# Optimization experiments

Hardware: AMD Instinct MI355X
Metric: run time of the kernel (lower is better)

The kernel has to match this reference:

```python
import jax, jax.numpy as jnp
import numpy as np

N, DIM, K = 131072, 64, 1024


def setup_inputs() -> dict:
    key = jax.random.key(0)
    kx, ke = jax.random.split(key)
    x = jax.random.normal(kx, (N, DIM), dtype=jnp.float32)
    # codebook buffer, initialized like uniform(-1/K, 1/K) in the original
    scale = 1.0 / K
    embedding = jax.random.uniform(ke, (K, DIM), dtype=jnp.float32, minval=-scale, maxval=scale)
    return {"x": x, "embedding": embedding}


def reference(x, embedding):
    # squared euclidean distances in fp32 (matches compute_distances)
    x32 = x.astype(jnp.float32)
    e32 = embedding.astype(jnp.float32)
    distances = (
        jnp.sum(x32 * x32, axis=1, keepdims=True)
        + jnp.sum(e32 * e32, axis=1)
        - 2.0 * jnp.einsum("nd,kd->nk", x32, e32)
    )
    indices = jnp.argmin(distances, axis=1)          # (N,)
    quantized = embedding[indices]                    # (N, DIM) codebook gather
    # commitment loss: mse(stop_grad(quantized), x)
    commitment_loss = jnp.mean((jax.lax.stop_gradient(quantized) - x) ** 2)
    # straight-through estimator
    quantized_st = x + jax.lax.stop_gradient(quantized - x)
    return quantized_st, indices, commitment_loss
```

## Files before the change

kernel.cpp:

```cpp
#include <hip/hip_runtime.h>
#include <hip/hip_bf16.h>

#define N_ROWS 131072
#define DIM 64
#define K_CODES 1024
#define NTILES 64
#define MARGIN 4e-5f
#define LIST_CAP 65536

typedef short short8 __attribute__((ext_vector_type(8)));
typedef float f32x4 __attribute__((ext_vector_type(4)));

__device__ __forceinline__ unsigned short f2bf(float f) {
    unsigned u = __float_as_uint(f);
    return (unsigned short)((u + 0x7fffu + ((u >> 16) & 1u)) >> 16);
}
__device__ __forceinline__ float bf2f(unsigned short h) {
    return __uint_as_float(((unsigned)h) << 16);
}

__device__ __forceinline__ float np_sq64(const float* __restrict__ v) {
    float xx[DIM];
    #pragma unroll
    for (int d = 0; d < DIM; ++d) xx[d] = v[d] * v[d];
    float r[8];
    #pragma unroll
    for (int j = 0; j < 8; ++j) r[j] = xx[j];
    #pragma unroll
    for (int i = 8; i < DIM; i += 8)
        #pragma unroll
        for (int j = 0; j < 8; ++j) r[j] = r[j] + xx[i + j];
    return ((r[0]+r[1]) + (r[2]+r[3])) + ((r[4]+r[5]) + (r[6]+r[7]));
}

__device__ __forceinline__ float np_dot64(const float* __restrict__ xv,
                                          const float* __restrict__ ek) {
    float a0 = 0.f, a1 = 0.f, a2 = 0.f, a3 = 0.f;
    #pragma unroll
    for (int c = 0; c < DIM; c += 16)
        #pragma unroll
        for (int b = 12; b >= 0; b -= 4) {
            const int d = c + b;
            a0 = a0 + xv[d+0] * ek[d+0];
            a1 = a1 + xv[d+1] * ek[d+1];
            a2 = a2 + xv[d+2] * ek[d+2];
            a3 = a3 + xv[d+3] * ek[d+3];
        }
    return (a0 + a1) + (a2 + a3);
}


__global__ void vq_prep(const float* __restrict__ emb, float* __restrict__ esq,
                        unsigned short* __restrict__ wsB,
                        unsigned int* __restrict__ cnt, float* __restrict__ loss) {
#pragma clang fp contract(off)
    const int t = blockIdx.x * blockDim.x + threadIdx.x;
    if (t == 0) { *cnt = 0u; *loss = 0.f; }
    const int k = t >> 2, c = t & 3;
    if (k >= K_CODES) return;
    const float* e = emb + (size_t)k * DIM;

    if (c == 0) esq[k] = np_sq64(e);

    const int off = (c & 1) * 32, sel = c >> 1;
    unsigned short val[32];
    #pragma unroll
    for (int j = 0; j < 32; ++j) {
        float v = e[off + j];
        unsigned short h = f2bf(v);
        val[j] = sel ? f2bf(v - bf2f(h)) : h;
    }
    const int tile = k >> 4, n = k & 15;
    #pragma unroll
    for (int g = 0; g < 4; ++g) {
        short8 s;
        #pragma unroll
        for (int j = 0; j < 8; ++j) s[j] = (short)val[g*8 + j];
        *reinterpret_cast<short8*>(wsB + ((size_t)((tile*4 + c)*64 + g*16 + n)) * 8) = s;
    }
}

__global__ __launch_bounds__(256, 2) void vq_mfma(const float* __restrict__ x,
        const float* __restrict__ emb, const float* __restrict__ esq,
        const unsigned short* __restrict__ wsB, float* __restrict__ out,
        unsigned int* __restrict__ cnt, unsigned int* __restrict__ list,
        float* __restrict__ loss) {
#pragma clang fp contract(off)
    const int tid = threadIdx.x;
    const int lane = tid & 63;
    const int w = tid >> 6;
    const int g = lane >> 4, res = lane & 15;
    const int rowbase = blockIdx.x * 256 + w * 64;

    short8 Ah[4][2], Al[4][2];
    #pragma unroll
    for (int rg = 0; rg < 4; ++rg) {
        const float* xr = x + (size_t)(rowbase + rg*16 + res) * DIM;
        #pragma unroll
        for (int h = 0; h < 2; ++h) {
            float4 v0 = *reinterpret_cast<const float4*>(xr + h*32 + g*8);
            float4 v1 = *reinterpret_cast<const float4*>(xr + h*32 + g*8 + 4);
            float xv[8] = {v0.x, v0.y, v0.z, v0.w, v1.x, v1.y, v1.z, v1.w};
            short8 sh, sl;
            #pragma unroll
            for (int j = 0; j < 8; ++j) {
                unsigned short hb = f2bf(xv[j]);
                sh[j] = (short)hb;
                sl[j] = (short)f2bf(xv[j] - bf2f(hb));
            }
            Ah[rg][h] = sh; Al[rg][h] = sl;
        }
    }

    float b1[16], b2[16], b3[16];
    const float FINF = __uint_as_float(0x7F800000u);
    #pragma unroll
    for (int s = 0; s < 16; ++s) { b1[s] = FINF; b2[s] = FINF; b3[s] = FINF; }

    auto loadB = [&](short8* Bd, int ct) {
        const unsigned short* bp = wsB + ((size_t)(ct*4)*64 + lane) * 8;
        #pragma unroll
        for (int c = 0; c < 4; ++c)
            Bd[c] = *reinterpret_cast<const short8*>(bp + (size_t)c * 64 * 8);
    };

    auto MF = [&](f32x4* acc, const short8* B) {
        #pragma unroll
        for (int rg = 0; rg < 4; ++rg) acc[rg] = f32x4{0.f, 0.f, 0.f, 0.f};
        #pragma unroll
        for (int rg = 0; rg < 4; ++rg)
            acc[rg] = __builtin_amdgcn_mfma_f32_16x16x32_bf16(Ah[rg][0], B[0], acc[rg], 0,0,0);
        #pragma unroll
        for (int rg = 0; rg < 4; ++rg)
            acc[rg] = __builtin_amdgcn_mfma_f32_16x16x32_bf16(Ah[rg][1], B[1], acc[rg], 0,0,0);
        #pragma unroll
        for (int rg = 0; rg < 4; ++rg)
            acc[rg] = __builtin_amdgcn_mfma_f32_16x16x32_bf16(Ah[rg][0], B[2], acc[rg], 0,0,0);
        #pragma unroll
        for (int rg = 0; rg < 4; ++rg)
            acc[rg] = __builtin_amdgcn_mfma_f32_16x16x32_bf16(Ah[rg][1], B[3], acc[rg], 0,0,0);
        #pragma unroll
        for (int rg = 0; rg < 4; ++rg)
            acc[rg] = __builtin_amdgcn_mfma_f32_16x16x32_bf16(Al[rg][0], B[0], acc[rg], 0,0,0);
        #pragma unroll
        for (int rg = 0; rg < 4; ++rg)
            acc[rg] = __builtin_amdgcn_mfma_f32_16x16x32_bf16(Al[rg][1], B[1], acc[rg], 0,0,0);
    };

    auto KY = [&](const f32x4* acc, float esqv, int ct) {
        const unsigned kcur = (unsigned)(ct*16 + res);
        #pragma unroll
        for (int rg = 0; rg < 4; ++rg) {
            #pragma unroll
            for (int r = 0; r < 4; ++r) {
                float v = fmaf(-2.0f, acc[rg][r], esqv);
                float key = __uint_as_float((__float_as_uint(v) & 0xFFFFFC00u) | kcur);
                const int s = rg*4 + r;
                float o1 = b1[s], o2 = b2[s];
                b3[s] = __builtin_amdgcn_fmed3f(key, o2, b3[s]);
                b2[s] = __builtin_amdgcn_fmed3f(key, o1, o2);
                b1[s] = fminf(o1, key);
            }
        }
    };

    short8 B0[4], B1[4];
    f32x4 accA[4], accB[4];
    float e0, e1;

    loadB(B0, 0); e0 = esq[res];
    loadB(B1, 1); e1 = esq[16 + res];
    MF(accA, B0);
    for (int p = 0; p < 31; ++p) {
        loadB(B0, 2*p + 2);
        MF(accB, B1);
        KY(accA, e0, 2*p);
        e0 = esq[(2*p + 2)*16 + res];
        loadB(B1, 2*p + 3);
        MF(accA, B0);
        KY(accB, e1, 2*p + 1);
        e1 = esq[(2*p + 3)*16 + res];
    }
    MF(accB, B1);
    KY(accA, e0, 62);
    KY(accB, e1, 63);

    #pragma unroll
    for (int m = 1; m < 16; m <<= 1) {
        #pragma unroll
        for (int s = 0; s < 16; ++s) {
            float oa1 = __shfl_xor(b1[s], m, 64);
            float oa2 = __shfl_xor(b2[s], m, 64);
            float oa3 = __shfl_xor(b3[s], m, 64);
            float m1 = fminf(b1[s], oa1);
            float m2 = fminf(fmaxf(b1[s], oa1), fminf(b2[s], oa2));
            float m3 = fminf(fminf(fmaxf(b1[s], oa2), fmaxf(b2[s], oa1)),
                             fminf(b3[s], oa3));
            b1[s] = m1; b2[s] = m2; b3[s] = m3;
        }
    }

    __shared__ float s_k1[256], s_k2[256], s_k3[256];
    __shared__ int s_idx[256];
    if (res == 0) {
        #pragma unroll
        for (int s = 0; s < 16; ++s) {
            const int rl = w*64 + (s >> 2)*16 + g*4 + (s & 3);
            s_k1[rl] = b1[s]; s_k2[rl] = b2[s]; s_k3[rl] = b3[s];
        }
    }
    __syncthreads();

    {
        const int row = blockIdx.x * 256 + tid;
        unsigned u1 = __float_as_uint(s_k1[tid]);
        unsigned u2 = __float_as_uint(s_k2[tid]);
        unsigned u3 = __float_as_uint(s_k3[tid]);
        float f1 = __uint_as_float(u1 & 0xFFFFFC00u);
        float f2 = __uint_as_float(u2 & 0xFFFFFC00u);
        float f3 = __uint_as_float(u3 & 0xFFFFFC00u);
        int idx;
        if (f3 - f1 < MARGIN) {
            unsigned slot = atomicAdd(cnt, 1u);
            if (slot < LIST_CAP) list[slot] = (unsigned)row;
            idx = -1;
        } else if (f2 - f1 < MARGIN) {
            const int ia = (int)(u1 & 0x3FFu), ib = (int)(u2 & 0x3FFu);
            float xv[DIM];
            const float4* xp = reinterpret_cast<const float4*>(x + (size_t)row * DIM);
            #pragma unroll
            for (int q = 0; q < 16; ++q) {
                float4 v = xp[q];
                xv[4*q+0] = v.x; xv[4*q+1] = v.y; xv[4*q+2] = v.z; xv[4*q+3] = v.w;
            }
            float xsq = np_sq64(xv);
            float ta = xsq + esq[ia];
            float da = ta - 2.0f * np_dot64(xv, emb + (size_t)ia * DIM);
            float tb = xsq + esq[ib];
            float db = tb - 2.0f * np_dot64(xv, emb + (size_t)ib * DIM);
            idx = (da < db) ? ia : ((db < da) ? ib : (ia < ib ? ia : ib));
        } else {
            idx = (int)(u1 & 0x3FFu);
        }
        s_idx[tid] = idx;
    }
    __syncthreads();

    float lsum = 0.f;
    #pragma unroll
    for (int pass = 0; pass < 2; ++pass) {
        const int rl = (tid >> 1) + pass * 128, half = tid & 1;
        const int row = blockIdx.x * 256 + rl;
        const int idx = s_idx[rl];
        if (idx >= 0) {
            const float* xr = x + (size_t)row * DIM + half*32;
            const float* qr = emb + (size_t)idx * DIM + half*32;
            float* orow = out + (size_t)row * DIM + half*32;
            #pragma unroll
            for (int i = 0; i < 8; ++i) {
                float4 xv = reinterpret_cast<const float4*>(xr)[i];
                float4 qv = reinterpret_cast<const float4*>(qr)[i];
                float df0 = qv.x - xv.x, df1 = qv.y - xv.y;
                float df2 = qv.z - xv.z, df3 = qv.w - xv.w;
                lsum = fmaf(df0, df0, lsum); lsum = fmaf(df1, df1, lsum);
                lsum = fmaf(df2, df2, lsum); lsum = fmaf(df3, df3, lsum);
                float4 o = {xv.x + df0, xv.y + df1, xv.z + df2, xv.w + df3};
                reinterpret_cast<float4*>(orow)[i] = o;
            }
            if (half == 0) out[(size_t)N_ROWS * DIM + row] = (float)idx;
        }
    }
    #pragma unroll
    for (int off = 32; off > 0; off >>= 1) lsum += __shfl_down(lsum, off, 64);
    if (lane == 0) atomicAdd(loss, lsum);
}

__global__ void vq_fixup(const float* __restrict__ x, const float* __restrict__ emb,
                         const float* __restrict__ esq,
                         const unsigned int* __restrict__ cnt,
                         const unsigned int* __restrict__ list,
                         float* __restrict__ out, float* __restrict__ loss) {
#pragma clang fp contract(off)
    const int lane = threadIdx.x & 63;
    const int wid = (blockIdx.x * blockDim.x + threadIdx.x) >> 6;
    const int nw = (256 * 256) >> 6;
    unsigned count = *cnt;
    if (count > LIST_CAP) count = LIST_CAP;
    for (unsigned i = wid; i < count; i += nw) {
        const int row = (int)list[i];
        float xv[DIM];
        const float4* xp = reinterpret_cast<const float4*>(x + (size_t)row * DIM);
        #pragma unroll
        for (int q = 0; q < 16; ++q) {
            float4 v = xp[q];
            xv[4*q+0] = v.x; xv[4*q+1] = v.y; xv[4*q+2] = v.z; xv[4*q+3] = v.w;
        }
        float xsq = np_sq64(xv);
        float best = INFINITY; int bidx = 0x7fffffff;
        for (int t = 0; t < K_CODES / 64; ++t) {
            const int k = lane + t * 64;
            float dot = np_dot64(xv, emb + (size_t)k * DIM);
            float tt = xsq + esq[k];
            float dist = tt - 2.0f * dot;
            if (dist < best) { best = dist; bidx = k; }
        }
        #pragma unroll
        for (int m = 1; m < 64; m <<= 1) {
            float ob = __shfl_xor(best, m, 64);
            int   oi = __shfl_xor(bidx, m, 64);
            if (ob < best || (ob == best && oi < bidx)) { best = ob; bidx = oi; }
        }
        const float xd = x[(size_t)row * DIM + lane];
        const float qd = emb[(size_t)bidx * DIM + lane];
        const float df = qd - xd;
        out[(size_t)row * DIM + lane] = xd + df;
        if (lane == 0) out[(size_t)N_ROWS * DIM + row] = (float)bidx;
        float l2 = df * df;
        #pragma unroll
        for (int off = 32; off > 0; off >>= 1) l2 += __shfl_down(l2, off, 64);
        if (lane == 0) atomicAdd(loss, l2);
    }
}

__global__ void vq_final(const float* __restrict__ loss_acc, float* __restrict__ out_loss) {
    if (threadIdx.x == 0 && blockIdx.x == 0)
        out_loss[0] = loss_acc[0] / (float)((size_t)N_ROWS * DIM);
}

extern "C" void kernel_launch(void* const* d_in, const int* in_sizes, int n_in,
                              void* d_out, int out_size, void* d_ws, size_t ws_size,
                              hipStream_t stream) {
    const float* x   = (const float*)d_in[0];
    const float* emb = (const float*)d_in[1];
    float* out = (float*)d_out;

    unsigned int* cnt  = (unsigned int*)d_ws;
    float* loss        = (float*)d_ws + 1;
    float* esq         = (float*)d_ws + 4;
    unsigned short* wsB = (unsigned short*)((char*)d_ws + 8192);
    unsigned int* list = (unsigned int*)((char*)d_ws + 270336);

    vq_prep<<<dim3(16), dim3(256), 0, stream>>>(emb, esq, wsB, cnt, loss);
    vq_mfma<<<dim3(N_ROWS / 256), dim3(256), 0, stream>>>(x, emb, esq, wsB, out,
                                                          cnt, list, loss);
    vq_fixup<<<dim3(256), dim3(256), 0, stream>>>(x, emb, esq, cnt, list, out, loss);
    vq_final<<<dim3(1), dim3(1), 0, stream>>>(loss, out + (size_t)N_ROWS * DIM + N_ROWS);
}
```

Before: 134.5 us.

## Split codebook across wave pairs and merge top-3 candidates in shared memory

Each block now handles 128 rows instead of 256. Each pair of waves shares one 64-row group, and each wave in the pair scans half of the codebook tiles. The per-half top-3 keys are merged through shared memory before the margin check and the output pass. This doubles the grid size and halves the serial MFMA loop length per wave, aiming for more parallelism and latency hiding. In exchange, each row's A fragments are loaded and split twice, and the block adds a merge step in shared memory.

Measured after the change: 152.9 us. +13.7%, slower.

```diff
diff --git a/kernel.cpp b/kernel.cpp
--- a/kernel.cpp
+++ b/kernel.cpp
@@ -5,6 +5,7 @@
 #define DIM 64
 #define K_CODES 1024
 #define NTILES 64
+#define HTILES 32
 #define MARGIN 4e-5f
 #define LIST_CAP 65536
 
@@ -89,8 +90,11 @@
     const int tid = threadIdx.x;
     const int lane = tid & 63;
     const int w = tid >> 6;
+    const int rowgrp = w >> 1;
+    const int khalf = w & 1;
     const int g = lane >> 4, res = lane & 15;
-    const int rowbase = blockIdx.x * 256 + w * 64;
+    const int rowbase = blockIdx.x * 128 + rowgrp * 64;
+    const int kb = khalf * HTILES;
 
     short8 Ah[4][2], Al[4][2];
     #pragma unroll
@@ -168,22 +172,22 @@
     f32x4 accA[4], accB[4];
     float e0, e1;
 
-    loadB(B0, 0); e0 = esq[res];
-    loadB(B1, 1); e1 = esq[16 + res];
+    loadB(B0, kb + 0); e0 = esq[(kb + 0)*16 + res];
+    loadB(B1, kb + 1); e1 = esq[(kb + 1)*16 + res];
     MF(accA, B0);
-    for (int p = 0; p < 31; ++p) {
-        loadB(B0, 2*p + 2);
+    for (int p = 0; p < 15; ++p) {
+        loadB(B0, kb + 2*p + 2);
         MF(accB, B1);
-        KY(accA, e0, 2*p);
-        e0 = esq[(2*p + 2)*16 + res];
-        loadB(B1, 2*p + 3);
+        KY(accA, e0, kb + 2*p);
+        e0 = esq[(kb + 2*p + 2)*16 + res];
+        loadB(B1, kb + 2*p + 3);
         MF(accA, B0);
-        KY(accB, e1, 2*p + 1);
-        e1 = esq[(2*p + 3)*16 + res];
+        KY(accB, e1, kb + 2*p + 1);
+        e1 = esq[(kb + 2*p + 3)*16 + res];
     }
     MF(accB, B1);
-    KY(accA, e0, 62);
-    KY(accB, e1, 63);
+    KY(accA, e0, kb + 30);
+    KY(accB, e1, kb + 31);
 
     #pragma unroll
     for (int m = 1; m < 16; m <<= 1) {
@@ -200,22 +204,27 @@
         }
     }
 
-    __shared__ float s_k1[256], s_k2[256], s_k3[256];
-    __shared__ int s_idx[256];
+    __shared__ float s_k1[2][128], s_k2[2][128], s_k3[2][128];
+    __shared__ int s_idx[128];
     if (res == 0) {
         #pragma unroll
         for (int s = 0; s < 16; ++s) {
-            const int rl = w*64 + (s >> 2)*16 + g*4 + (s & 3);
-            s_k1[rl] = b1[s]; s_k2[rl] = b2[s]; s_k3[rl] = b3[s];
+            const int rl = rowgrp*64 + (s >> 2)*16 + g*4 + (s & 3);
+            s_k1[khalf][rl] = b1[s]; s_k2[khalf][rl] = b2[s]; s_k3[khalf][rl] = b3[s];
         }
     }
     __syncthreads();
 
-    {
-        const int row = blockIdx.x * 256 + tid;
-        unsigned u1 = __float_as_uint(s_k1[tid]);
-        unsigned u2 = __float_as_uint(s_k2[tid]);
-        unsigned u3 = __float_as_uint(s_k3[tid]);
+    if (tid < 128) {
+        const int row = blockIdx.x * 128 + tid;
+        float a1 = s_k1[0][tid], a2 = s_k2[0][tid], a3 = s_k3[0][tid];
+        float c1 = s_k1[1][tid], c2 = s_k2[1][tid], c3 = s_k3[1][tid];
+        float k1 = fminf(a1, c1);
+        float k2 = fminf(fmaxf(a1, c1), fminf(a2, c2));
+        float k3 = fminf(fminf(fmaxf(a1, c2), fmaxf(a2, c1)), fminf(a3, c3));
+        unsigned u1 = __float_as_uint(k1);
+        unsigned u2 = __float_as_uint(k2);
+        unsigned u3 = __float_as_uint(k3);
         float f1 = __uint_as_float(u1 & 0xFFFFFC00u);
         float f2 = __uint_as_float(u2 & 0xFFFFFC00u);
         float f3 = __uint_as_float(u3 & 0xFFFFFC00u);
@@ -247,10 +256,9 @@
     __syncthreads();
 
     float lsum = 0.f;
-    #pragma unroll
-    for (int pass = 0; pass < 2; ++pass) {
-        const int rl = (tid >> 1) + pass * 128, half = tid & 1;
-        const int row = blockIdx.x * 256 + rl;
+    {
+        const int rl = tid >> 1, half = tid & 1;
+        const int row = blockIdx.x * 128 + rl;
         const int idx = s_idx[rl];
         if (idx >= 0) {
             const float* xr = x + (size_t)row * DIM + half*32;
@@ -341,7 +349,7 @@
     unsigned int* list = (unsigned int*)((char*)d_ws + 270336);
 
     vq_prep<<<dim3(16), dim3(256), 0, stream>>>(emb, esq, wsB, cnt, loss);
-    vq_mfma<<<dim3(N_ROWS / 256), dim3(256), 0, stream>>>(x, emb, esq, wsB, out,
+    vq_mfma<<<dim3(N_ROWS / 128), dim3(256), 0, stream>>>(x, emb, esq, wsB, out,
                                                           cnt, list, loss);
     vq_fixup<<<dim3(256), dim3(256), 0, stream>>>(x, emb, esq, cnt, list, out, loss);
     vq_final<<<dim3(1), dim3(1), 0, stream>>>(loss, out + (size_t)N_ROWS * DIM + N_ROWS);
```

## Deepen B-operand prefetch to four buffers, raise MFMA priority, use nontemporal stores

Applied to the files above, without the earlier changes.

The codebook tile pipeline goes from double to quadruple buffering of B fragments. The first four tiles are issued before the x rows are converted, so global load latency has more independent work to hide behind. MFMA sequences are wrapped in s_setprio to favour the matrix issue over other waves' work. Output stores become nontemporal to avoid polluting cache. The extra B registers raise VGPR pressure under launch_bounds(256,2), which could force spills or lower occupancy.

After: 134.2 us. Within noise of the previous version (-0.2%).

```diff
diff --git a/kernel.cpp b/kernel.cpp
--- a/kernel.cpp
+++ b/kernel.cpp
@@ -91,6 +91,17 @@
     const int w = tid >> 6;
     const int g = lane >> 4, res = lane & 15;
     const int rowbase = blockIdx.x * 256 + w * 64;
+
+    auto loadB = [&](short8* Bd, int ct) {
+        const unsigned short* bp = wsB + ((size_t)(ct*4)*64 + lane) * 8;
+        #pragma unroll
+        for (int c = 0; c < 4; ++c)
+            Bd[c] = *reinterpret_cast<const short8*>(bp + (size_t)c * 64 * 8);
+    };
+
+    short8 B0[4], B1[4], B2[4], B3[4];
+    loadB(B0, 0); loadB(B1, 1); loadB(B2, 2); loadB(B3, 3);
+    float e0 = esq[res], e1 = esq[16 + res];
 
     short8 Ah[4][2], Al[4][2];
     #pragma unroll
@@ -117,14 +128,8 @@
     #pragma unroll
     for (int s = 0; s < 16; ++s) { b1[s] = FINF; b2[s] = FINF; b3[s] = FINF; }
 
-    auto loadB = [&](short8* Bd, int ct) {
-        const unsigned short* bp = wsB + ((size_t)(ct*4)*64 + lane) * 8;
-        #pragma unroll
-        for (int c = 0; c < 4; ++c)
-            Bd[c] = *reinterpret_cast<const short8*>(bp + (size_t)c * 64 * 8);
-    };
-
     auto MF = [&](f32x4* acc, const short8* B) {
+        __builtin_amdgcn_s_setprio(1);
         #pragma unroll
         for (int rg = 0; rg < 4; ++rg) acc[rg] = f32x4{0.f, 0.f, 0.f, 0.f};
         #pragma unroll
@@ -145,6 +150,7 @@
         #pragma unroll
         for (int rg = 0; rg < 4; ++rg)
             acc[rg] = __builtin_amdgcn_mfma_f32_16x16x32_bf16(Al[rg][1], B[1], acc[rg], 0,0,0);
+        __builtin_amdgcn_s_setprio(0);
     };
 
     auto KY = [&](const f32x4* acc, float esqv, int ct) {
@@ -164,24 +170,28 @@
         }
     };
 
-    short8 B0[4], B1[4];
     f32x4 accA[4], accB[4];
-    float e0, e1;
-
-    loadB(B0, 0); e0 = esq[res];
-    loadB(B1, 1); e1 = esq[16 + res];
     MF(accA, B0);
-    for (int p = 0; p < 31; ++p) {
-        loadB(B0, 2*p + 2);
+    for (int p = 0; p < 15; ++p) {
+        const int t = 4 * p;
+        loadB(B0, t + 4);
         MF(accB, B1);
-        KY(accA, e0, 2*p);
-        e0 = esq[(2*p + 2)*16 + res];
-        loadB(B1, 2*p + 3);
+        KY(accA, e0, t);      e0 = esq[(t + 2) * 16 + res];
+        loadB(B1, t + 5);
+        MF(accA, B2);
+        KY(accB, e1, t + 1);  e1 = esq[(t + 3) * 16 + res];
+        loadB(B2, t + 6);
+        MF(accB, B3);
+        KY(accA, e0, t + 2);  e0 = esq[(t + 4) * 16 + res];
+        loadB(B3, t + 7);
         MF(accA, B0);
-        KY(accB, e1, 2*p + 1);
-        e1 = esq[(2*p + 3)*16 + res];
+        KY(accB, e1, t + 3);  e1 = esq[(t + 5) * 16 + res];
     }
     MF(accB, B1);
+    KY(accA, e0, 60);  e0 = esq[62 * 16 + res];
+    MF(accA, B2);
+    KY(accB, e1, 61);  e1 = esq[63 * 16 + res];
+    MF(accB, B3);
     KY(accA, e0, 62);
     KY(accB, e1, 63);
 
@@ -264,10 +274,11 @@
                 float df2 = qv.z - xv.z, df3 = qv.w - xv.w;
                 lsum = fmaf(df0, df0, lsum); lsum = fmaf(df1, df1, lsum);
                 lsum = fmaf(df2, df2, lsum); lsum = fmaf(df3, df3, lsum);
-                float4 o = {xv.x + df0, xv.y + df1, xv.z + df2, xv.w + df3};
-                reinterpret_cast<float4*>(orow)[i] = o;
+                f32x4 o = {xv.x + df0, xv.y + df1, xv.z + df2, xv.w + df3};
+                __builtin_nontemporal_store(o, reinterpret_cast<f32x4*>(orow) + i);
             }
-            if (half == 0) out[(size_t)N_ROWS * DIM + row] = (float)idx;
+            if (half == 0)
+                __builtin_nontemporal_store((float)idx, &out[(size_t)N_ROWS * DIM + row]);
         }
     }
     #pragma unroll
```
